# Performance work log

Hardware: AMD Instinct MI355X
Metric: run time of the kernel (lower is better)

The kernel has to match this reference:

```python
import jax, jax.numpy as jnp
import numpy as np

L, H, P = 16384, 1024, 512  # seq len, model width, state size (conj_sym: P = ssm_size//2)
DT_MIN, DT_MAX = 1e-3, 1e-1
STEP_RESCALE = 1.0


def setup_inputs() -> dict:
    key = jax.random.key(0)
    ks = jax.random.split(key, 7)
    input_sequence = jax.random.normal(ks[0], (L, H), dtype=jnp.float32)
    # Lambda: stable diagonal (Re < 0), like DPLR-HiPPO (Re = -0.5, spread imag parts)
    Lambda_re = -0.5 - jax.random.uniform(ks[1], (P,), dtype=jnp.float32)
    Lambda_im = 10.0 * jax.random.normal(ks[2], (P,), dtype=jnp.float32)
    # B (P,H,2) and C (H,P,2): real/imag stacked parameterization
    B = jax.random.normal(ks[3], (P, H, 2), dtype=jnp.float32) / np.float32(np.sqrt(H))
    C = jax.random.normal(ks[4], (H, P, 2), dtype=jnp.float32) / np.float32(np.sqrt(P))
    D = jax.random.normal(ks[5], (H,), dtype=jnp.float32)
    log_step = (jax.random.uniform(ks[6], (P, 1), dtype=jnp.float32)
                * (np.log(DT_MAX) - np.log(DT_MIN)) + np.log(DT_MIN)).astype(jnp.float32)
    return {"input_sequence": input_sequence, "Lambda_re": Lambda_re,
            "Lambda_im": Lambda_im, "B": B, "C": C, "D": D, "log_step": log_step}


def _binop(q_i, q_j):
    # diagonal linear recurrence composition; elementwise, so works on stacked arrays
    A_i, b_i = q_i
    A_j, b_j = q_j
    return (A_j * A_i, A_j * b_i + b_j)


def reference(input_sequence, Lambda_re, Lambda_im, B, C, D, log_step):
    Lambda = Lambda_re + 1j * Lambda_im                      # (P,) complex64
    B_tilde = B[..., 0] + 1j * B[..., 1]                     # (P,H)
    C_tilde = C[..., 0] + 1j * C[..., 1]                     # (H,P)
    Delta = STEP_RESCALE * jnp.exp(log_step[:, 0])           # (P,)
    # ZOH discretization
    Lambda_bar = jnp.exp(Lambda * Delta)                     # (P,)
    B_bar = ((Lambda_bar - 1.0) / Lambda)[:, None] * B_tilde # (P,H)
    # per-step scan elements
    Lambda_elements = jnp.broadcast_to(Lambda_bar, (input_sequence.shape[0], P))
    Bu_elements = jnp.einsum('lh,ph->lp', input_sequence, B_bar)  # (L,P) complex
    _, xs = jax.lax.associative_scan(_binop, (Lambda_elements, Bu_elements))
    # conj_sym readout: 2 * Re(C x)
    ys = 2.0 * jnp.einsum('lp,hp->lh', xs, C_tilde).real     # (L,H) float32
    return ys + input_sequence * D
```

## Files before the change

kernel.cpp:

```cpp
#include <hip/hip_runtime.h>
#include <math.h>

#define LL 16384
#define HH 1024
#define PP 512
#define NP2 1024
#define CHUNK 64
#define NCHUNK 256
#define BM 128
#define BN 128
#define BK 32

typedef unsigned short u16;
typedef __attribute__((ext_vector_type(8))) short bf16x8;
typedef __attribute__((ext_vector_type(4))) float f32x4;

__device__ __forceinline__ u16 f2bf(float f) {
    unsigned u = __float_as_uint(f);
    unsigned r = 0x7fffu + ((u >> 16) & 1u);
    return (u16)((u + r) >> 16);
}
__device__ __forceinline__ float bf2f(u16 x) {
    return __uint_as_float(((unsigned)x) << 16);
}

__device__ __forceinline__ void gload_lds16(const void* g, void* l) {
    __builtin_amdgcn_global_load_lds(
        (const __attribute__((address_space(1))) unsigned int*)g,
        (__attribute__((address_space(3))) unsigned int*)l, 16, 0, 0);
}

__global__ void k_setup(const float* __restrict__ lre, const float* __restrict__ lim,
                        const float* __restrict__ logstep,
                        float* __restrict__ gre, float* __restrict__ gim,
                        float* __restrict__ lbre, float* __restrict__ lbim,
                        float* __restrict__ ltre, float* __restrict__ ltim) {
    int p = threadIdx.x;
    if (p >= PP) return;
    float dt = expf(logstep[p]);
    float ar = lre[p], ai = lim[p];
    float e = expf(ar * dt);
    float s, c;
    sincosf(ai * dt, &s, &c);
    float Lr = e * c, Li = e * s;
    lbre[p] = Lr; lbim[p] = Li;
    float nr = Lr - 1.0f, ni = Li;
    float den = ar * ar + ai * ai;
    gre[p] = (nr * ar + ni * ai) / den;
    gim[p] = (ni * ar - nr * ai) / den;
    float tr = Lr, ti = Li;
    for (int i = 0; i < 6; i++) {
        float rr = tr * tr - ti * ti;
        float mm = 2.0f * tr * ti;
        tr = rr; ti = mm;
    }
    ltre[p] = tr; ltim[p] = ti;
}

__global__ void k_prep2(const float* __restrict__ B,
                        const float* __restrict__ gre, const float* __restrict__ gim,
                        const float* __restrict__ C,
                        u16* __restrict__ bb, u16* __restrict__ cp) {
    if (blockIdx.x < 2048) {
        int t = blockIdx.x * 256 + threadIdx.x;
        int p = t >> 10;
        float2 b = ((const float2*)B)[t];
        float gr = gre[p], gi = gim[p];
        bb[t] = f2bf(gr * b.x - gi * b.y);
        bb[(size_t)PP * HH + t] = f2bf(gr * b.y + gi * b.x);
    } else {
        int t = (blockIdx.x - 2048) * 256 + threadIdx.x;
        int h = t >> 9, p = t & 511;
        float2 c = ((const float2*)C)[t];
        cp[(size_t)h * NP2 + p] = f2bf(c.x);
        cp[(size_t)h * NP2 + PP + p] = f2bf(-c.y);
    }
}

__global__ void k_cvt(const float* __restrict__ s, u16* __restrict__ d) {
    size_t i = ((size_t)blockIdx.x * 256 + threadIdx.x) * 4;
    float4 v = *(const float4*)&s[i];
    unsigned lo = (unsigned)f2bf(v.x) | ((unsigned)f2bf(v.y) << 16);
    unsigned hi = (unsigned)f2bf(v.z) | ((unsigned)f2bf(v.w) << 16);
    *(uint2*)&d[i] = make_uint2(lo, hi);
}

template<int FUSE>
__global__ __launch_bounds__(256) void k_gemm(
        const u16* __restrict__ A, const u16* __restrict__ Bt,
        void* __restrict__ outp, const int K,
        const u16* __restrict__ ubf, const float* __restrict__ Din) {
    __shared__ u16 smem[2 * BM * BK];
    u16* lA = smem;
    u16* lB = smem + BM * BK;
    const int b = blockIdx.x;
    const int xcd = b & 7, s = b >> 3;
    const int m0 = (xcd * 16 + (s >> 3)) * BM;
    const int n0 = (s & 7) * BN;
    const int N = 8 * BN;
    const int t = threadIdx.x;
    const int lane = t & 63, wid = t >> 6;
    const int wm = (wid >> 1) * 64, wn = (wid & 1) * 64;
    const int frow = lane & 15, quad = lane >> 4;

    f32x4 acc[4][4];
    #pragma unroll
    for (int i = 0; i < 4; i++)
        #pragma unroll
        for (int j = 0; j < 4; j++) acc[i][j] = (f32x4){0.f, 0.f, 0.f, 0.f};

    const int sr = t >> 2, slot = t & 3;
    const int seg = slot ^ ((sr >> 1) & 3);
    const u16* gA = A + (size_t)(m0 + sr) * K + seg * 8;
    const u16* gB = Bt + (size_t)(n0 + sr) * K + seg * 8;
    u16* dA = &lA[sr * BK + slot * 8];
    u16* dB = &lB[sr * BK + slot * 8];

    for (int k0 = 0; k0 < K; k0 += BK) {
        __syncthreads();
        gload_lds16(gA + k0, dA);
        gload_lds16(gA + (size_t)64 * K + k0, dA + 64 * BK);
        gload_lds16(gB + k0, dB);
        gload_lds16(gB + (size_t)64 * K + k0, dB + 64 * BK);
        __syncthreads();
        bf16x8 av[4], bv[4];
        #pragma unroll
        for (int i = 0; i < 4; i++) {
            const int r = wm + i * 16 + frow;
            av[i] = *(const bf16x8*)&lA[r * BK + (quad ^ ((r >> 1) & 3)) * 8];
        }
        #pragma unroll
        for (int j = 0; j < 4; j++) {
            const int r = wn + j * 16 + frow;
            bv[j] = *(const bf16x8*)&lB[r * BK + (quad ^ ((r >> 1) & 3)) * 8];
        }
        #pragma unroll
        for (int i = 0; i < 4; i++)
            #pragma unroll
            for (int j = 0; j < 4; j++)
                acc[i][j] = __builtin_amdgcn_mfma_f32_16x16x32_bf16(
                    av[i], bv[j], acc[i][j], 0, 0, 0);
    }

    if (FUSE) {
        float* Cout = (float*)outp;
        #pragma unroll
        for (int i = 0; i < 4; i++) {
            const int row = m0 + wm + i * 16 + quad * 4;
            #pragma unroll
            for (int j = 0; j < 4; j++) {
                const int col = n0 + wn + j * 16 + frow;
                const float dv = Din[col];
                f32x4 v = acc[i][j];
                #pragma unroll
                for (int r = 0; r < 4; r++) {
                    const size_t o = (size_t)(row + r) * N + col;
                    Cout[o] = 2.0f * v[r] + bf2f(ubf[o]) * dv;
                }
            }
        }
    } else {
        u16* Cb = (u16*)outp;
        const int half = wm >> 6;
        __syncthreads();
        #pragma unroll
        for (int i = 0; i < 4; i++) {
            #pragma unroll
            for (int j = 0; j < 4; j++) {
                f32x4 v = acc[i][j];
                #pragma unroll
                for (int r = 0; r < 4; r++)
                    smem[half * 2048 + (quad * 4 + r) * 128 + wn + j * 16 + frow]
                        = f2bf(v[r]);
            }
            __syncthreads();
            #pragma unroll
            for (int c = 0; c < 2; c++) {
                const int fe = (t + c * 256) * 8;
                const int hh = fe >> 11, rem = fe & 2047;
                const int qr = rem >> 7, cb = rem & 127;
                const int row = m0 + hh * 64 + i * 16 + qr;
                *(uint4*)&Cb[(size_t)row * N + n0 + cb] = *(const uint4*)&smem[fe];
            }
            __syncthreads();
        }
    }
}

__global__ void k_scan1(const u16* __restrict__ bu,
                        const float* __restrict__ lbre, const float* __restrict__ lbim,
                        float* __restrict__ fr, float* __restrict__ fi) {
    int p = blockIdx.x * 256 + threadIdx.x;
    int c = blockIdx.y;
    float ar = lbre[p], ai = lbim[p];
    float xr = 0.f, xi = 0.f;
    const u16* b = bu + (size_t)c * CHUNK * NP2 + p;
    for (int j = 0; j < CHUNK; j++) {
        float br = bf2f(b[0]), bi = bf2f(b[PP]);
        float nr = ar * xr - ai * xi + br;
        float ni = ar * xi + ai * xr + bi;
        xr = nr; xi = ni;
        b += NP2;
    }
    fr[c * PP + p] = xr;
    fi[c * PP + p] = xi;
}

__global__ __launch_bounds__(256) void k_scan2(
        const float* __restrict__ fr, const float* __restrict__ fi,
        const float* __restrict__ ltre, const float* __restrict__ ltim,
        float* __restrict__ cr, float* __restrict__ ci) {
    __shared__ float Ar[NCHUNK], Ai[NCHUNK], br[NCHUNK], bi[NCHUNK];
    const int p = blockIdx.x;
    const int c = threadIdx.x;
    const float lr = ltre[p], li = ltim[p];
    Ar[c] = lr; Ai[c] = li;
    br[c] = fr[c * PP + p];
    bi[c] = fi[c * PP + p];
    __syncthreads();
    #pragma unroll
    for (int d = 1; d < NCHUNK; d <<= 1) {
        float pAr = 0.f, pAi = 0.f, pbr = 0.f, pbi = 0.f;
        const bool has = (c >= d);
        if (has) { pAr = Ar[c-d]; pAi = Ai[c-d]; pbr = br[c-d]; pbi = bi[c-d]; }
        float cAr = Ar[c], cAi = Ai[c], cbr = br[c], cbi = bi[c];
        __syncthreads();
        if (has) {
            Ar[c] = cAr * pAr - cAi * pAi;
            Ai[c] = cAr * pAi + cAi * pAr;
            br[c] = cAr * pbr - cAi * pbi + cbr;
            bi[c] = cAr * pbi + cAi * pbr + cbi;
        }
        __syncthreads();
    }
    cr[c * PP + p] = (c == 0) ? 0.f : br[c-1];
    ci[c * PP + p] = (c == 0) ? 0.f : bi[c-1];
}

__global__ void k_scan3(u16* __restrict__ bu,
                        const float* __restrict__ lbre, const float* __restrict__ lbim,
                        const float* __restrict__ cr, const float* __restrict__ ci) {
    int p = blockIdx.x * 256 + threadIdx.x;
    int c = blockIdx.y;
    float ar = lbre[p], ai = lbim[p];
    float xr = cr[c * PP + p], xi = ci[c * PP + p];
    u16* b = bu + (size_t)c * CHUNK * NP2 + p;
    for (int j = 0; j < CHUNK; j++) {
        float br = bf2f(b[0]), bi = bf2f(b[PP]);
        float nr = ar * xr - ai * xi + br;
        float ni = ar * xi + ai * xr + bi;
        xr = nr; xi = ni;
        b[0] = f2bf(xr);
        b[PP] = f2bf(xi);
        b += NP2;
    }
}

extern "C" void kernel_launch(void* const* d_in, const int* in_sizes, int n_in,
                              void* d_out, int out_size, void* d_ws, size_t ws_size,
                              hipStream_t stream) {
    const float* u       = (const float*)d_in[0];
    const float* lre     = (const float*)d_in[1];
    const float* lim     = (const float*)d_in[2];
    const float* B       = (const float*)d_in[3];
    const float* C       = (const float*)d_in[4];
    const float* D       = (const float*)d_in[5];
    const float* logstep = (const float*)d_in[6];
    float* out = (float*)d_out;

    float* w = (float*)d_ws;
    float* gre  = w;
    float* gim  = w + 512;
    float* lbre = w + 1024;
    float* lbim = w + 1536;
    float* ltre = w + 2048;
    float* ltim = w + 2560;
    float* fr   = w + 4096;
    float* fi   = fr + NCHUNK * PP;
    float* cr   = fi + NCHUNK * PP;
    float* ci   = cr + NCHUNK * PP;
    u16*   bub  = (u16*)(w + (1 << 20));
    u16*   ub   = bub + (size_t)LL * NP2;
    u16*   bb   = ub + (size_t)LL * HH;
    u16*   cp   = bb + (size_t)NP2 * HH;

    k_setup<<<1, 512, 0, stream>>>(lre, lim, logstep, gre, gim, lbre, lbim, ltre, ltim);
    k_prep2<<<4096, 256, 0, stream>>>(B, gre, gim, C, bb, cp);
    k_cvt<<<(LL * HH) / 1024, 256, 0, stream>>>(u, ub);
    k_gemm<0><<<(NP2 / BN) * (LL / BM), 256, 0, stream>>>(ub, bb, bub, HH, nullptr, nullptr);
    k_scan1<<<dim3(PP / 256, NCHUNK), 256, 0, stream>>>(bub, lbre, lbim, fr, fi);
    k_scan2<<<PP, NCHUNK, 0, stream>>>(fr, fi, ltre, ltim, cr, ci);
    k_scan3<<<dim3(PP / 256, NCHUNK), 256, 0, stream>>>(bub, lbre, lbim, cr, ci);
    k_gemm<1><<<(HH / BN) * (LL / BM), 256, 0, stream>>>(bub, cp, out, NP2, ub, D);
}
```

Measured before the change: 269.0 us.

## Fuse chunk-local scan into Bu GEMM epilogue with interleaved re/im layout

Interleaves the real and imaginary parts of B_bar rows and C columns so that each Bu output column pair holds (re, im) for one state. The first GEMM epilogue then runs the per-chunk local scan from LDS and writes the chunk-final states, which removes the separate k_scan1 pass over the full Bu array. k_scan3 now reads and writes packed 32-bit re/im words. GEMM BK is raised to 64 with an 8-way XOR swizzle. The epilogue scan uses only 128 threads running a serial recurrence, which may lengthen the GEMM tail.

```diff
diff --git a/kernel.cpp b/kernel.cpp
--- a/kernel.cpp
+++ b/kernel.cpp
@@ -9,7 +9,7 @@
 #define NCHUNK 256
 #define BM 128
 #define BN 128
-#define BK 32
+#define BK 64
 
 typedef unsigned short u16;
 typedef __attribute__((ext_vector_type(8))) short bf16x8;
@@ -63,17 +63,17 @@
                         u16* __restrict__ bb, u16* __restrict__ cp) {
     if (blockIdx.x < 2048) {
         int t = blockIdx.x * 256 + threadIdx.x;
-        int p = t >> 10;
+        int p = t >> 10, h = t & 1023;
         float2 b = ((const float2*)B)[t];
         float gr = gre[p], gi = gim[p];
-        bb[t] = f2bf(gr * b.x - gi * b.y);
-        bb[(size_t)PP * HH + t] = f2bf(gr * b.y + gi * b.x);
+        bb[(size_t)(2 * p) * HH + h]     = f2bf(gr * b.x - gi * b.y);
+        bb[(size_t)(2 * p + 1) * HH + h] = f2bf(gr * b.y + gi * b.x);
     } else {
         int t = (blockIdx.x - 2048) * 256 + threadIdx.x;
         int h = t >> 9, p = t & 511;
         float2 c = ((const float2*)C)[t];
-        cp[(size_t)h * NP2 + p] = f2bf(c.x);
-        cp[(size_t)h * NP2 + PP + p] = f2bf(-c.y);
+        cp[(size_t)h * NP2 + 2 * p]     = f2bf(c.x);
+        cp[(size_t)h * NP2 + 2 * p + 1] = f2bf(-c.y);
     }
 }
 
@@ -89,7 +89,9 @@
 __global__ __launch_bounds__(256) void k_gemm(
         const u16* __restrict__ A, const u16* __restrict__ Bt,
         void* __restrict__ outp, const int K,
-        const u16* __restrict__ ubf, const float* __restrict__ Din) {
+        const u16* __restrict__ ubf, const float* __restrict__ Din,
+        const float* __restrict__ lbre, const float* __restrict__ lbim,
+        float* __restrict__ frO, float* __restrict__ fiO) {
     __shared__ u16 smem[2 * BM * BK];
     u16* lA = smem;
     u16* lB = smem + BM * BK;
@@ -102,6 +104,7 @@
     const int lane = t & 63, wid = t >> 6;
     const int wm = (wid >> 1) * 64, wn = (wid & 1) * 64;
     const int frow = lane & 15, quad = lane >> 4;
+    const int swz = frow & 7;
 
     f32x4 acc[4][4];
     #pragma unroll
@@ -109,8 +112,8 @@
         #pragma unroll
         for (int j = 0; j < 4; j++) acc[i][j] = (f32x4){0.f, 0.f, 0.f, 0.f};
 
-    const int sr = t >> 2, slot = t & 3;
-    const int seg = slot ^ ((sr >> 1) & 3);
+    const int sr = t >> 3, slot = t & 7;
+    const int seg = slot ^ (sr & 7);
     const u16* gA = A + (size_t)(m0 + sr) * K + seg * 8;
     const u16* gB = Bt + (size_t)(n0 + sr) * K + seg * 8;
     u16* dA = &lA[sr * BK + slot * 8];
@@ -118,28 +121,30 @@
 
     for (int k0 = 0; k0 < K; k0 += BK) {
         __syncthreads();
-        gload_lds16(gA + k0, dA);
-        gload_lds16(gA + (size_t)64 * K + k0, dA + 64 * BK);
-        gload_lds16(gB + k0, dB);
-        gload_lds16(gB + (size_t)64 * K + k0, dB + 64 * BK);
-        __syncthreads();
-        bf16x8 av[4], bv[4];
-        #pragma unroll
-        for (int i = 0; i < 4; i++) {
-            const int r = wm + i * 16 + frow;
-            av[i] = *(const bf16x8*)&lA[r * BK + (quad ^ ((r >> 1) & 3)) * 8];
-        }
-        #pragma unroll
-        for (int j = 0; j < 4; j++) {
-            const int r = wn + j * 16 + frow;
-            bv[j] = *(const bf16x8*)&lB[r * BK + (quad ^ ((r >> 1) & 3)) * 8];
-        }
-        #pragma unroll
-        for (int i = 0; i < 4; i++)
+        #pragma unroll
+        for (int g = 0; g < 4; g++) {
+            gload_lds16(gA + (size_t)(32 * g) * K + k0, dA + 32 * g * BK);
+            gload_lds16(gB + (size_t)(32 * g) * K + k0, dB + 32 * g * BK);
+        }
+        __syncthreads();
+        #pragma unroll
+        for (int kk = 0; kk < 2; kk++) {
+            bf16x8 av[4], bv[4];
+            #pragma unroll
+            for (int i = 0; i < 4; i++)
+                av[i] = *(const bf16x8*)&lA[(wm + i * 16 + frow) * BK
+                                            + (((kk << 2) | quad) ^ swz) * 8];
             #pragma unroll
             for (int j = 0; j < 4; j++)
-                acc[i][j] = __builtin_amdgcn_mfma_f32_16x16x32_bf16(
-                    av[i], bv[j], acc[i][j], 0, 0, 0);
+                bv[j] = *(const bf16x8*)&lB[(wn + j * 16 + frow) * BK
+                                            + (((kk << 2) | quad) ^ swz) * 8];
+            #pragma unroll
+            for (int i = 0; i < 4; i++)
+                #pragma unroll
+                for (int j = 0; j < 4; j++)
+                    acc[i][j] = __builtin_amdgcn_mfma_f32_16x16x32_bf16(
+                        av[i], bv[j], acc[i][j], 0, 0, 0);
+        }
     }
 
     if (FUSE) {
@@ -161,7 +166,12 @@
         }
     } else {
         u16* Cb = (u16*)outp;
+        unsigned* sm32 = (unsigned*)smem;
         const int half = wm >> 6;
+        const int sq = t & 63, sh = t >> 6;
+        const int sp = (n0 >> 1) + sq;
+        float sar = 0.f, sai = 0.f, sxr = 0.f, sxi = 0.f;
+        if (t < 128) { sar = lbre[sp]; sai = lbim[sp]; }
         __syncthreads();
         #pragma unroll
         for (int i = 0; i < 4; i++) {
@@ -182,28 +192,25 @@
                 const int row = m0 + hh * 64 + i * 16 + qr;
                 *(uint4*)&Cb[(size_t)row * N + n0 + cb] = *(const uint4*)&smem[fe];
             }
+            if (t < 128) {
+                #pragma unroll
+                for (int r = 0; r < 16; r++) {
+                    unsigned v = sm32[sh * 1024 + r * 64 + sq];
+                    float br = bf2f((u16)(v & 0xffff));
+                    float bi = bf2f((u16)(v >> 16));
+                    float nr = sar * sxr - sai * sxi + br;
+                    float ni = sar * sxi + sai * sxr + bi;
+                    sxr = nr; sxi = ni;
+                }
+            }
             __syncthreads();
         }
-    }
-}
-
-__global__ void k_scan1(const u16* __restrict__ bu,
-                        const float* __restrict__ lbre, const float* __restrict__ lbim,
-                        float* __restrict__ fr, float* __restrict__ fi) {
-    int p = blockIdx.x * 256 + threadIdx.x;
-    int c = blockIdx.y;
-    float ar = lbre[p], ai = lbim[p];
-    float xr = 0.f, xi = 0.f;
-    const u16* b = bu + (size_t)c * CHUNK * NP2 + p;
-    for (int j = 0; j < CHUNK; j++) {
-        float br = bf2f(b[0]), bi = bf2f(b[PP]);
-        float nr = ar * xr - ai * xi + br;
-        float ni = ar * xi + ai * xr + bi;
-        xr = nr; xi = ni;
-        b += NP2;
-    }
-    fr[c * PP + p] = xr;
-    fi[c * PP + p] = xi;
+        if (t < 128) {
+            const int chunk = (m0 >> 6) + sh;
+            frO[chunk * PP + sp] = sxr;
+            fiO[chunk * PP + sp] = sxi;
+        }
+    }
 }
 
 __global__ __launch_bounds__(256) void k_scan2(
@@ -237,22 +244,23 @@
     ci[c * PP + p] = (c == 0) ? 0.f : bi[c-1];
 }
 
-__global__ void k_scan3(u16* __restrict__ bu,
+__global__ void k_scan3(unsigned* __restrict__ bu,
                         const float* __restrict__ lbre, const float* __restrict__ lbim,
                         const float* __restrict__ cr, const float* __restrict__ ci) {
     int p = blockIdx.x * 256 + threadIdx.x;
     int c = blockIdx.y;
     float ar = lbre[p], ai = lbim[p];
     float xr = cr[c * PP + p], xi = ci[c * PP + p];
-    u16* b = bu + (size_t)c * CHUNK * NP2 + p;
+    unsigned* b = bu + (size_t)c * CHUNK * PP + p;
     for (int j = 0; j < CHUNK; j++) {
-        float br = bf2f(b[0]), bi = bf2f(b[PP]);
+        unsigned v = *b;
+        float br = bf2f((u16)(v & 0xffff));
+        float bi = bf2f((u16)(v >> 16));
         float nr = ar * xr - ai * xi + br;
         float ni = ar * xi + ai * xr + bi;
         xr = nr; xi = ni;
-        b[0] = f2bf(xr);
-        b[PP] = f2bf(xi);
-        b += NP2;
+        *b = (unsigned)f2bf(xr) | ((unsigned)f2bf(xi) << 16);
+        b += PP;
     }
 }
 
@@ -287,9 +295,11 @@
     k_setup<<<1, 512, 0, stream>>>(lre, lim, logstep, gre, gim, lbre, lbim, ltre, ltim);
     k_prep2<<<4096, 256, 0, stream>>>(B, gre, gim, C, bb, cp);
     k_cvt<<<(LL * HH) / 1024, 256, 0, stream>>>(u, ub);
-    k_gemm<0><<<(NP2 / BN) * (LL / BM), 256, 0, stream>>>(ub, bb, bub, HH, nullptr, nullptr);
-    k_scan1<<<dim3(PP / 256, NCHUNK), 256, 0, stream>>>(bub, lbre, lbim, fr, fi);
+    k_gemm<0><<<(NP2 / BN) * (LL / BM), 256, 0, stream>>>(
+        ub, bb, bub, HH, nullptr, nullptr, lbre, lbim, fr, fi);
     k_scan2<<<PP, NCHUNK, 0, stream>>>(fr, fi, ltre, ltim, cr, ci);
-    k_scan3<<<dim3(PP / 256, NCHUNK), 256, 0, stream>>>(bub, lbre, lbim, cr, ci);
-    k_gemm<1><<<(HH / BN) * (LL / BM), 256, 0, stream>>>(bub, cp, out, NP2, ub, D);
-}
+    k_scan3<<<dim3(PP / 256, NCHUNK), 256, 0, stream>>>(
+        (unsigned*)bub, lbre, lbim, cr, ci);
+    k_gemm<1><<<(HH / BN) * (LL / BM), 256, 0, stream>>>(
+        bub, cp, out, NP2, ub, D, nullptr, nullptr, nullptr, nullptr);
+}
```

Result: faster. 248.3 us (-7.7%).
